# Kernel tuning notes

Hardware: AMD Instinct MI355X
Metric: run time of the kernel (lower is better)

Reference implementation:

```python
import jax, jax.numpy as jnp
import numpy as np

M_DIM = 1024
N_HEADS = 16
H_DIM = M_DIM // N_HEADS
B, S_DEC, S_ENC = 2, 2048, 2048
NEG = -1e9
LN_EPS = 1e-5


def _layernorm(x, g, b):
    mu = jnp.mean(x, axis=-1, keepdims=True)
    var = jnp.mean(jnp.square(x - mu), axis=-1, keepdims=True)
    return (x - mu) * jax.lax.rsqrt(var + LN_EPS) * g + b


def _mha(q_in, kv_in, Wq, bq, Wk, bk, Wv, bv, causal):
    # Wq/Wk/Wv: [H, m_dim, h_dim]; stacked equivalent of per-head nn.Linear
    q = jnp.einsum('bsm,hmd->bhsd', q_in, Wq) + bq[:, None, :]
    k = jnp.einsum('bsm,hmd->bhsd', kv_in, Wk) + bk[:, None, :]
    v = jnp.einsum('bsm,hmd->bhsd', kv_in, Wv) + bv[:, None, :]
    scores = jnp.einsum('bhqd,bhkd->bhqk', q, k) / jnp.sqrt(jnp.asarray(H_DIM, q.dtype))
    if causal:
        sq, sk = scores.shape[-2], scores.shape[-1]
        mask = jnp.tril(jnp.ones((sq, sk), dtype=bool))
        scores = jnp.where(mask, scores, jnp.asarray(NEG, scores.dtype))
    attn = jax.nn.softmax(scores, axis=-1)
    o = jnp.einsum('bhqk,bhkd->bhqd', attn, v)
    bsz, h, sq, d = o.shape
    # concat order: head-major along last dim, same as torch.cat over heads
    return o.transpose(0, 2, 1, 3).reshape(bsz, sq, h * d)


def setup_inputs() -> dict:
    key = jax.random.key(0)
    ks = jax.random.split(key, 32)
    s = 1.0 / np.sqrt(M_DIM)
    s2 = 1.0 / np.sqrt(2 * M_DIM)
    d = {
        'input': jax.random.normal(ks[0], (B, S_DEC, M_DIM), jnp.float32),
        'encoder_out': jax.random.normal(ks[1], (B, S_ENC, M_DIM), jnp.float32),
        # self-attention heads (stacked)
        'Wq1': jax.random.normal(ks[2], (N_HEADS, M_DIM, H_DIM), jnp.float32) * s,
        'bq1': jnp.zeros((N_HEADS, H_DIM), jnp.float32),
        'Wk1': jax.random.normal(ks[3], (N_HEADS, M_DIM, H_DIM), jnp.float32) * s,
        'bk1': jnp.zeros((N_HEADS, H_DIM), jnp.float32),
        'Wv1': jax.random.normal(ks[4], (N_HEADS, M_DIM, H_DIM), jnp.float32) * s,
        'bv1': jnp.zeros((N_HEADS, H_DIM), jnp.float32),
        'Wo1': jax.random.normal(ks[5], (M_DIM, M_DIM), jnp.float32) * s,
        'bo1': jnp.zeros((M_DIM,), jnp.float32),
        'ln1_g': jnp.ones((M_DIM,), jnp.float32),
        'ln1_b': jnp.zeros((M_DIM,), jnp.float32),
        # cross-attention heads (stacked)
        'Wq2': jax.random.normal(ks[6], (N_HEADS, M_DIM, H_DIM), jnp.float32) * s,
        'bq2': jnp.zeros((N_HEADS, H_DIM), jnp.float32),
        'Wk2': jax.random.normal(ks[7], (N_HEADS, M_DIM, H_DIM), jnp.float32) * s,
        'bk2': jnp.zeros((N_HEADS, H_DIM), jnp.float32),
        'Wv2': jax.random.normal(ks[8], (N_HEADS, M_DIM, H_DIM), jnp.float32) * s,
        'bv2': jnp.zeros((N_HEADS, H_DIM), jnp.float32),
        'Wo2': jax.random.normal(ks[9], (M_DIM, M_DIM), jnp.float32) * s,
        'bo2': jnp.zeros((M_DIM,), jnp.float32),
        'ln2_g': jnp.ones((M_DIM,), jnp.float32),
        'ln2_b': jnp.zeros((M_DIM,), jnp.float32),
        # FFN (expansion factor 2, per source)
        'W_ff1': jax.random.normal(ks[10], (M_DIM, 2 * M_DIM), jnp.float32) * s,
        'b_ff1': jnp.zeros((2 * M_DIM,), jnp.float32),
        'W_ff2': jax.random.normal(ks[11], (2 * M_DIM, M_DIM), jnp.float32) * s2,
        'b_ff2': jnp.zeros((M_DIM,), jnp.float32),
        'ln3_g': jnp.ones((M_DIM,), jnp.float32),
        'ln3_b': jnp.zeros((M_DIM,), jnp.float32),
    }
    return d


def reference(input, encoder_out,
              Wq1, bq1, Wk1, bk1, Wv1, bv1, Wo1, bo1, ln1_g, ln1_b,
              Wq2, bq2, Wk2, bk2, Wv2, bv2, Wo2, bo2, ln2_g, ln2_b,
              W_ff1, b_ff1, W_ff2, b_ff2, ln3_g, ln3_b):
    # masked self-attention (dropout = identity in eval)
    sa = _mha(input, input, Wq1, bq1, Wk1, bk1, Wv1, bv1, causal=True)
    sa = sa @ Wo1 + bo1
    out1 = _layernorm(sa + input, ln1_g, ln1_b)
    # cross-attention
    ca = _mha(out1, encoder_out, Wq2, bq2, Wk2, bk2, Wv2, bv2, causal=False)
    ca = ca @ Wo2 + bo2
    out1 = _layernorm(out1 + ca, ln2_g, ln2_b)
    # FFN
    ff = jax.nn.relu(out1 @ W_ff1 + b_ff1) @ W_ff2 + b_ff2
    out = _layernorm(ff + out1, ln3_g, ln3_b)
    return out
```

## Files before the change

### kernel.cpp

```cpp
#include <hip/hip_runtime.h>
#include <math.h>

#define B_ 2
#define S_ 2048
#define M_ 1024
#define H_ 16
#define D_ 64
#define R_ (B_*S_)

typedef __attribute__((ext_vector_type(8))) short short8v;
typedef __attribute__((ext_vector_type(4))) float float4v;

__device__ __forceinline__ float4 ld4(const float* p) {
    return *(const float4* __restrict__)p;
}

__device__ __forceinline__ ushort f2bf(float f) {
    union { float f; unsigned u; } x; x.f = f;
    unsigned u = x.u + 0x7fffu + ((x.u >> 16) & 1u);
    return (ushort)(u >> 16);
}
__device__ __forceinline__ float bf2f(ushort s) {
    union { unsigned u; float f; } x; x.u = ((unsigned)s) << 16; return x.f;
}
__device__ __forceinline__ unsigned cvtpk(float lo, float hi) {
    unsigned r;
    asm("v_cvt_pk_bf16_f32 %0, %1, %2" : "=v"(r) : "v"(lo), "v"(hi));
    return r;
}
#if __has_builtin(__builtin_amdgcn_exp2f)
__device__ __forceinline__ float fexp2(float x) { return __builtin_amdgcn_exp2f(x); }
#else
__device__ __forceinline__ float fexp2(float x) { return exp2f(x); }
#endif
#if __has_builtin(__builtin_amdgcn_rcpf)
__device__ __forceinline__ float frcp(float x) { return __builtin_amdgcn_rcpf(x); }
#else
__device__ __forceinline__ float frcp(float x) { return 1.f / x; }
#endif
__device__ __forceinline__ float4v mfma16(short8v a, short8v b, float4v c) {
    return __builtin_amdgcn_mfma_f32_16x16x32_bf16(a, b, c, 0, 0, 0);
}
__device__ __forceinline__ void glds16(const void* g, void* l) {
    __builtin_amdgcn_global_load_lds(
        (const __attribute__((address_space(1))) void*)g,
        (__attribute__((address_space(3))) void*)l, 16, 0, 0);
}

__global__ __launch_bounds__(256) void cast2_k(const float* __restrict__ a,
                                               const float* __restrict__ b,
                                               ushort* __restrict__ oa,
                                               ushort* __restrict__ ob) {
    size_t u = (size_t)blockIdx.x * 256 + threadIdx.x;
    const float* in; ushort* out;
    if (u < (1u << 20)) { in = a; out = oa; }
    else { u -= (1u << 20); in = b; out = ob; }
    float4 v = ld4(in + u * 4);
    ushort4 o = { f2bf(v.x), f2bf(v.y), f2bf(v.z), f2bf(v.w) };
    *(ushort4*)&out[u * 4] = o;
}

__global__ __launch_bounds__(256) void biasp_k(
    const float* __restrict__ q1, const float* __restrict__ k1,
    const float* __restrict__ v1, const float* __restrict__ k2,
    const float* __restrict__ v2, const float* __restrict__ q2,
    float* __restrict__ dst, float SCv) {
    const int seg = blockIdx.x >> 2;
    const int li = (blockIdx.x & 3) * 256 + threadIdx.x;
    const float* s; int off; float sc;
    switch (seg) {
        case 0: s = q1; off = 0;    sc = SCv; break;
        case 1: s = k1; off = 1024; sc = 1.f; break;
        case 2: s = v1; off = 2048; sc = 1.f; break;
        case 3: s = k2; off = 4096; sc = 1.f; break;
        case 4: s = v2; off = 5120; sc = 1.f; break;
        default: s = q2; off = 8192; sc = SCv; break;
    }
    dst[off + li] = s[li] * sc;
}

__global__ __launch_bounds__(256) void wtransH_k(
    const float* __restrict__ s0, const float* __restrict__ s1,
    const float* __restrict__ s2, const float* __restrict__ s3,
    const float* __restrict__ s4, const float* __restrict__ s5,
    ushort* __restrict__ oQKV1, ushort* __restrict__ oQ2,
    ushort* __restrict__ oKV2, float SCv) {
    __shared__ float t[32][33];
    const int z = blockIdx.z, s6 = z >> 4, h = z & 15;
    const float* srcs[6] = { s0, s1, s2, s3, s4, s5 };
    const float* ib = srcs[s6] + (size_t)h * 1024 * 64;
    ushort* ob;
    if (s6 < 3)       ob = oQKV1 + (size_t)s6 * (1024 * 1024) + (size_t)h * (64 * 1024);
    else if (s6 == 3) ob = oQ2 + (size_t)h * (64 * 1024);
    else              ob = oKV2 + (size_t)(s6 - 4) * (1024 * 1024) + (size_t)h * (64 * 1024);
    const float scale = (s6 == 0 || s6 == 3) ? SCv : 1.f;
    const int k0 = blockIdx.y * 32, n0 = blockIdx.x * 32;
    const int tx = threadIdx.x & 31, ty = threadIdx.x >> 5;
    #pragma unroll
    for (int i = 0; i < 4; ++i)
        t[ty + i * 8][tx] = ib[(size_t)(k0 + ty + i * 8) * 64 + n0 + tx];
    __syncthreads();
    #pragma unroll
    for (int i = 0; i < 4; ++i)
        ob[(size_t)(n0 + ty + i * 8) * 1024 + k0 + tx] = f2bf(t[tx][ty + i * 8] * scale);
}

__global__ __launch_bounds__(256) void wtrans_k(const float* __restrict__ inA,
                                                const float* __restrict__ inB,
                                                ushort* __restrict__ outA,
                                                ushort* __restrict__ outB,
                                                int K, int N) {
    __shared__ float t[32][33];
    const float* ib = blockIdx.z ? inB : inA;
    ushort* ob = blockIdx.z ? outB : outA;
    const int k0 = blockIdx.y * 32, n0 = blockIdx.x * 32;
    const int tx = threadIdx.x & 31, ty = threadIdx.x >> 5;
    #pragma unroll
    for (int i = 0; i < 4; ++i)
        t[ty + i * 8][tx] = ib[(size_t)(k0 + ty + i * 8) * N + n0 + tx];
    __syncthreads();
    #pragma unroll
    for (int i = 0; i < 4; ++i)
        ob[(size_t)(n0 + ty + i * 8) * K + k0 + tx] = f2bf(t[tx][ty + i * 8]);
}

template<int TM, int TN, int BK, int OUTMODE, int ACT>
__global__ __launch_bounds__(256) void gemm_bf16_k(
    const ushort* __restrict__ A, const ushort* __restrict__ Bt,
    const float* __restrict__ bias, void* __restrict__ C,
    ushort* __restrict__ Cvt, int matV, int N, int K)
{
    constexpr int NI = TM / 32;
    constexpr int NJ = TN / 32;
    constexpr int KS = BK / 32;
    constexpr int CHR = BK / 8;
    __shared__ __align__(16) ushort At[TM * BK];
    __shared__ __align__(16) ushort Bts[TN * BK];
    const int tid = threadIdx.x, lane = tid & 63, w = tid >> 6;
    const int wm = w >> 1, wn = w & 1;
    const int q = lane & 15, g = lane >> 4;
    const int m0 = blockIdx.y * TM, n0 = blockIdx.x * TN;

    float4v acc[NI][NJ];
    #pragma unroll
    for (int i = 0; i < NI; ++i)
        #pragma unroll
        for (int j = 0; j < NJ; ++j) acc[i][j] = (float4v){0.f, 0.f, 0.f, 0.f};

    for (int k0 = 0; k0 < K; k0 += BK) {
        #pragma unroll
        for (int t = 0; t < TM * CHR / 256; ++t) {
            const int cb = (w * (TM * CHR / 256) + t) * 64;
            const int c = cb + lane;
            const int row = c / CHR, kc = (c % CHR) ^ (row & (CHR - 1));
            glds16(&A[(size_t)(m0 + row) * K + k0 + kc * 8], &At[cb * 8]);
        }
        #pragma unroll
        for (int t = 0; t < TN * CHR / 256; ++t) {
            const int cb = (w * (TN * CHR / 256) + t) * 64;
            const int c = cb + lane;
            const int row = c / CHR, kc = (c % CHR) ^ (row & (CHR - 1));
            glds16(&Bt[(size_t)(n0 + row) * K + k0 + kc * 8], &Bts[cb * 8]);
        }
        __syncthreads();
        #pragma unroll
        for (int ks = 0; ks < KS; ++ks) {
            short8v af[NI], bf[NJ];
            #pragma unroll
            for (int i = 0; i < NI; ++i) {
                const int row = wm * (TM / 2) + i * 16 + q;
                af[i] = *(const short8v*)((const char*)At +
                        row * (BK * 2) + (((ks * 4 + g) ^ (q & (CHR - 1))) << 4));
            }
            #pragma unroll
            for (int j = 0; j < NJ; ++j) {
                const int row = wn * (TN / 2) + j * 16 + q;
                bf[j] = *(const short8v*)((const char*)Bts +
                        row * (BK * 2) + (((ks * 4 + g) ^ (q & (CHR - 1))) << 4));
            }
            #pragma unroll
            for (int i = 0; i < NI; ++i)
                #pragma unroll
                for (int j = 0; j < NJ; ++j)
                    acc[i][j] = mfma16(af[i], bf[j], acc[i][j]);
        }
        __syncthreads();
    }

    float bcol[NJ];
    #pragma unroll
    for (int j = 0; j < NJ; ++j) bcol[j] = bias[n0 + wn * (TN / 2) + j * 16 + q];

    #pragma unroll
    for (int i = 0; i < NI; ++i) {
        const int rowg0 = m0 + wm * (TM / 2) + i * 16 + g * 4;
        #pragma unroll
        for (int j = 0; j < NJ; ++j) {
            const int colg = n0 + wn * (TN / 2) + j * 16 + q;
            float v[4];
            #pragma unroll
            for (int r = 0; r < 4; ++r) {
                v[r] = acc[i][j][r] + bcol[j];
                if (ACT) v[r] = fmaxf(v[r], 0.f);
            }
            if (OUTMODE == 0) {
                #pragma unroll
                for (int r = 0; r < 4; ++r)
                    ((float*)C)[(size_t)(rowg0 + r) * N + colg] = v[r];
            } else if (OUTMODE == 1) {
                #pragma unroll
                for (int r = 0; r < 4; ++r)
                    ((ushort*)C)[(size_t)(rowg0 + r) * N + colg] = f2bf(v[r]);
            } else {
                const int mat = colg >> 10, h = (colg >> 6) & 15, d = colg & 63;
                const int bb = rowg0 >> 11, s0 = rowg0 & 2047;
                if (mat == matV) {
                    uint2 pv;
                    pv.x = cvtpk(v[0], v[1]);
                    pv.y = cvtpk(v[2], v[3]);
                    *(uint2*)&Cvt[((size_t)(bb * H_ + h) * D_ + d) * S_ + s0] = pv;
                } else {
                    #pragma unroll
                    for (int r = 0; r < 4; ++r)
                        ((ushort*)C)[((((size_t)(mat * B_ + bb) * H_ + h) * S_) + s0 + r) * D_ + d] = f2bf(v[r]);
                }
            }
        }
    }
}

template<int CAUSAL>
__global__ __launch_bounds__(256, 2) void fattn_k(
    const ushort* __restrict__ Qg, const ushort* __restrict__ Kg,
    const ushort* __restrict__ VTg, ushort* __restrict__ Og, int Skv)
{
    __shared__ __align__(16) ushort Kt[2][64 * 64];
    __shared__ __align__(16) ushort Vt[2][64 * 64];
    __shared__ __align__(16) ushort Pt[128 * 64];
    const int tid = threadIdx.x, lane = tid & 63, w = tid >> 6;
    const int g = lane >> 4, q = lane & 15;
    const int id = blockIdx.x;
    const int bh = id & 31;
    const int qb = CAUSAL ? (15 - (id >> 5)) : (id >> 5);
    const int q0b = qb * 128;
    const int q0w = q0b + w * 32;

    const int c0 = tid, c1 = tid + 256;
    const ushort* kS0 = Kg + ((size_t)bh * Skv + (c0 >> 3)) * 64 + (((c0 & 7) ^ ((c0 >> 3) & 7)) * 8);
    const ushort* kS1 = Kg + ((size_t)bh * Skv + (c1 >> 3)) * 64 + (((c1 & 7) ^ ((c1 >> 3) & 7)) * 8);
    const ushort* vS0 = VTg + ((size_t)bh * 64 + (c0 >> 3)) * (size_t)Skv + (((c0 & 7) ^ ((c0 >> 3) & 7)) * 8);
    const ushort* vS1 = VTg + ((size_t)bh * 64 + (c1 >> 3)) * (size_t)Skv + (((c1 & 7) ^ ((c1 >> 3) & 7)) * 8);

#define STAGE(nb) do { \
        glds16(kS0, &Kt[nb][(w * 64) * 8]); \
        glds16(kS1, &Kt[nb][(256 + w * 64) * 8]); \
        glds16(vS0, &Vt[nb][(w * 64) * 8]); \
        glds16(vS1, &Vt[nb][(256 + w * 64) * 8]); \
        kS0 += 64 * 64; kS1 += 64 * 64; vS0 += 64; vS1 += 64; } while (0)

    short8v qf[2][2];
    #pragma unroll
    for (int h2 = 0; h2 < 2; ++h2)
        #pragma unroll
        for (int kf = 0; kf < 2; ++kf)
            qf[h2][kf] = *(const short8v*)&Qg[((size_t)bh * S_ + q0w + h2 * 16 + q) * 64 + kf * 32 + g * 8];

    const int swz = (g ^ (q & 7)) << 4;
    const int ktB = q * 128 + swz;
    const int vtB = q * 128 + swz;
    const int pfB0 = (w * 32 + q) * 128 + swz;
    const int poB0 = (w * 32 + q) * 128 +
                     ((((g >> 1) ^ (q & 7)) << 4) | ((g & 1) << 3));

    float4v oacc[4][2];
    #pragma unroll
    for (int d2 = 0; d2 < 4; ++d2)
        #pragma unroll
        for (int h2 = 0; h2 < 2; ++h2) oacc[d2][h2] = (float4v){0.f, 0.f, 0.f, 0.f};
    float m_[2] = {-1e30f, -1e30f}, l_[2] = {0.f, 0.f};

    const int ktiles = CAUSAL ? (2 * qb + 2) : (Skv >> 6);
    int cur = 0;

    STAGE(0);
    __syncthreads();

    for (int kt = 0; kt < ktiles; ++kt) {
        if (kt + 1 < ktiles) STAGE(cur ^ 1);
        const char* ktp = (const char*)Kt + cur * 8192;
        const char* vtp = (const char*)Vt + cur * 8192;
        const int kv0 = kt * 64;

        float4v st[2][4];
        __builtin_amdgcn_s_setprio(1);
        #pragma unroll
        for (int kvf = 0; kvf < 4; ++kvf) {
            short8v k0 = *(const short8v*)(ktp + (ktB + kvf * 2048));
            short8v k1 = *(const short8v*)(ktp + ((ktB + kvf * 2048) ^ 64));
            #pragma unroll
            for (int h2 = 0; h2 < 2; ++h2) {
                st[h2][kvf] = mfma16(k0, qf[h2][0], (float4v){0.f, 0.f, 0.f, 0.f});
                st[h2][kvf] = mfma16(k1, qf[h2][1], st[h2][kvf]);
            }
        }
        __builtin_amdgcn_s_setprio(0);

        if (CAUSAL && kv0 + 63 > q0b) {
            #pragma unroll
            for (int h2 = 0; h2 < 2; ++h2) {
                const int qg_ = q0w + h2 * 16 + q;
                #pragma unroll
                for (int kvf = 0; kvf < 4; ++kvf)
                    #pragma unroll
                    for (int r = 0; r < 4; ++r)
                        if (kv0 + kvf * 16 + g * 4 + r > qg_) st[h2][kvf][r] = -1e9f;
            }
        }

        #pragma unroll
        for (int h2 = 0; h2 < 2; ++h2) {
            float mA[4];
            #pragma unroll
            for (int kvf = 0; kvf < 4; ++kvf)
                mA[kvf] = fmaxf(fmaxf(st[h2][kvf][0], st[h2][kvf][1]),
                                fmaxf(st[h2][kvf][2], st[h2][kvf][3]));
            float mx = fmaxf(fmaxf(mA[0], mA[1]), fmaxf(mA[2], mA[3]));
            mx = fmaxf(mx, __shfl_xor(mx, 16));
            mx = fmaxf(mx, __shfl_xor(mx, 32));

            if (!__all(mx <= m_[h2])) {
                const float nm = fmaxf(m_[h2], mx);
                const float f = fexp2(m_[h2] - nm);
                l_[h2] *= f;
                #pragma unroll
                for (int d2 = 0; d2 < 4; ++d2) oacc[d2][h2] = oacc[d2][h2] * f;
                m_[h2] = nm;
            }

            float sA[4];
            #pragma unroll
            for (int kvf = 0; kvf < 4; ++kvf) {
                #pragma unroll
                for (int r = 0; r < 4; ++r) st[h2][kvf][r] = fexp2(st[h2][kvf][r] - m_[h2]);
                sA[kvf] = (st[h2][kvf][0] + st[h2][kvf][1]) + (st[h2][kvf][2] + st[h2][kvf][3]);
            }
            l_[h2] += (sA[0] + sA[1]) + (sA[2] + sA[3]);

            #pragma unroll
            for (int kvf = 0; kvf < 4; ++kvf) {
                uint2 pv;
                pv.x = cvtpk(st[h2][kvf][0], st[h2][kvf][1]);
                pv.y = cvtpk(st[h2][kvf][2], st[h2][kvf][3]);
                *(uint2*)((char*)Pt + ((poB0 + h2 * 2048) ^ (kvf << 5))) = pv;
            }
        }

        short8v pf[2][2];
        #pragma unroll
        for (int kf = 0; kf < 2; ++kf)
            #pragma unroll
            for (int h2 = 0; h2 < 2; ++h2)
                pf[kf][h2] = *(const short8v*)((const char*)Pt + ((pfB0 + h2 * 2048) ^ (kf << 6)));
        __builtin_amdgcn_s_setprio(1);
        #pragma unroll
        for (int df = 0; df < 4; ++df) {
            #pragma unroll
            for (int kf = 0; kf < 2; ++kf) {
                short8v vfr = *(const short8v*)(vtp + ((vtB + df * 2048) ^ (kf << 6)));
                #pragma unroll
                for (int h2 = 0; h2 < 2; ++h2)
                    oacc[df][h2] = mfma16(vfr, pf[kf][h2], oacc[df][h2]);
            }
        }
        __builtin_amdgcn_s_setprio(0);

        __syncthreads();
        cur ^= 1;
    }
#undef STAGE

    #pragma unroll
    for (int h2 = 0; h2 < 2; ++h2) {
        float lr = l_[h2];
        lr += __shfl_xor(lr, 16);
        lr += __shfl_xor(lr, 32);
        const float inv = frcp(lr);
        const int qr = w * 32 + h2 * 16 + q;
        #pragma unroll
        for (int df = 0; df < 4; ++df) {
            uint2 ov;
            ov.x = cvtpk(oacc[df][h2][0] * inv, oacc[df][h2][1] * inv);
            ov.y = cvtpk(oacc[df][h2][2] * inv, oacc[df][h2][3] * inv);
            *(uint2*)((char*)Pt + qr * 128 +
                      ((((2 * df + (g >> 1)) ^ (q & 7)) << 4) | ((g & 1) << 3))) = ov;
        }
    }
    __syncthreads();
    const int b = bh >> 4, h = bh & 15;
    #pragma unroll
    for (int t = 0; t < 4; ++t) {
        const int c = t * 256 + tid;
        const int qrow = c >> 3, ch = c & 7;
        short8v v = *(const short8v*)((char*)Pt + qrow * 128 + ((ch ^ (qrow & 7)) << 4));
        *(short8v*)&Og[((size_t)(b * S_ + q0b + qrow)) * M_ + h * 64 + ch * 8] = v;
    }
}

template<int EMITB>
__global__ __launch_bounds__(256) void ln_k(
    const ushort* __restrict__ X, const float* __restrict__ Rz,
    const float* __restrict__ g, const float* __restrict__ be,
    float* __restrict__ outf, ushort* __restrict__ outb)
{
    __shared__ float red[8];
    const int row = blockIdx.x, tid = threadIdx.x;
    const int lane = tid & 63, w = tid >> 6;

    ushort4 xu = *(const ushort4*)&X[(size_t)row * M_ + tid * 4];
    float4 rr = ld4(Rz + (size_t)row * M_ + tid * 4);
    float4 x = make_float4(bf2f(xu.x) + rr.x, bf2f(xu.y) + rr.y,
                           bf2f(xu.z) + rr.z, bf2f(xu.w) + rr.w);

    float sm = x.x + x.y + x.z + x.w;
    #pragma unroll
    for (int off = 1; off < 64; off <<= 1) sm += __shfl_xor(sm, off);
    if (lane == 0) red[w] = sm;
    __syncthreads();
    const float mean = (red[0] + red[1] + red[2] + red[3]) * (1.f / M_);

    x.x -= mean; x.y -= mean; x.z -= mean; x.w -= mean;
    float vs = x.x * x.x + x.y * x.y + x.z * x.z + x.w * x.w;
    #pragma unroll
    for (int off = 1; off < 64; off <<= 1) vs += __shfl_xor(vs, off);
    if (lane == 0) red[4 + w] = vs;
    __syncthreads();
    const float var = (red[4] + red[5] + red[6] + red[7]) * (1.f / M_);
    const float rs = rsqrtf(var + 1e-5f);

    float4 gg = ld4(g + tid * 4), bb = ld4(be + tid * 4);
    float4 y = make_float4(x.x * rs * gg.x + bb.x, x.y * rs * gg.y + bb.y,
                           x.z * rs * gg.z + bb.z, x.w * rs * gg.w + bb.w);
    *(float4*)(outf + (size_t)row * M_ + tid * 4) = y;
    if (EMITB) {
        ushort4 ob = { f2bf(y.x), f2bf(y.y), f2bf(y.z), f2bf(y.w) };
        *(ushort4*)&outb[(size_t)row * M_ + tid * 4] = ob;
    }
}

extern "C" void kernel_launch(void* const* d_in, const int* in_sizes, int n_in,
                              void* d_out, int out_size, void* d_ws, size_t ws_size,
                              hipStream_t stream)
{
    const float* input = (const float*)d_in[0];
    const float* enc   = (const float*)d_in[1];
    const float* Wq1 = (const float*)d_in[2];  const float* bq1 = (const float*)d_in[3];
    const float* Wk1 = (const float*)d_in[4];  const float* bk1 = (const float*)d_in[5];
    const float* Wv1 = (const float*)d_in[6];  const float* bv1 = (const float*)d_in[7];
    const float* Wo1 = (const float*)d_in[8];  const float* bo1 = (const float*)d_in[9];
    const float* ln1g = (const float*)d_in[10]; const float* ln1b = (const float*)d_in[11];
    const float* Wq2 = (const float*)d_in[12]; const float* bq2 = (const float*)d_in[13];
    const float* Wk2 = (const float*)d_in[14]; const float* bk2 = (const float*)d_in[15];
    const float* Wv2 = (const float*)d_in[16]; const float* bv2 = (const float*)d_in[17];
    const float* Wo2 = (const float*)d_in[18]; const float* bo2 = (const float*)d_in[19];
    const float* ln2g = (const float*)d_in[20]; const float* ln2b = (const float*)d_in[21];
    const float* Wf1 = (const float*)d_in[22]; const float* bf1 = (const float*)d_in[23];
    const float* Wf2 = (const float*)d_in[24]; const float* bf2 = (const float*)d_in[25];
    const float* ln3g = (const float*)d_in[26]; const float* ln3b = (const float*)d_in[27];

    const float SC = 0.18033688011112042f;

    char* W = (char*)d_ws;
    #define OFS(mb) ((void*)(W + (size_t)(mb) * 1024 * 1024))
    ushort* x0b    = (ushort*)OFS(0);
    ushort* encb   = (ushort*)OFS(8);
    ushort* WqkvT1 = (ushort*)OFS(16);
    ushort* Wo1T   = (ushort*)OFS(22);
    ushort* Wq2T   = (ushort*)OFS(24);
    ushort* WkvT2  = (ushort*)OFS(26);
    ushort* Wo2T   = (ushort*)OFS(30);
    ushort* Wf1T   = (ushort*)OFS(32);
    ushort* Wf2T   = (ushort*)OFS(36);
    float*  biasQKV1 = (float*)OFS(40);
    float*  biasKV2  = (float*)((char*)OFS(40) + 16384);
    float*  biasQ2   = (float*)((char*)OFS(40) + 32768);
    ushort* QKV1   = (ushort*)OFS(41);
    ushort* VT1    = (ushort*)OFS(65);
    ushort* att1b  = (ushort*)OFS(73);
    ushort* o1b    = (ushort*)OFS(81);
    float*  out1f  = (float*)OFS(41);
    ushort* out1b  = (ushort*)OFS(57);
    ushort* Q2     = (ushort*)OFS(65);
    ushort* KV2    = (ushort*)OFS(73);
    ushort* VT2    = (ushort*)OFS(0);
    ushort* att2b  = (ushort*)OFS(8);
    ushort* o2b    = (ushort*)OFS(65);
    float*  out2f  = (float*)OFS(73);
    ushort* out2b  = (ushort*)OFS(0);
    ushort* ff1b   = (ushort*)OFS(41);
    ushort* ff2b   = (ushort*)OFS(57);
    float*  out    = (float*)d_out;
    const size_t MAT = (size_t)B_ * H_ * S_ * D_;

    dim3 blk(256);

    cast2_k<<<8192, blk, 0, stream>>>(input, enc, x0b, encb);
    biasp_k<<<24, blk, 0, stream>>>(bq1, bk1, bv1, bk2, bv2, bq2, biasQKV1, SC);
    wtransH_k<<<dim3(2, 32, 96), blk, 0, stream>>>(Wq1, Wk1, Wv1, Wq2, Wk2, Wv2,
                                                   WqkvT1, Wq2T, WkvT2, SC);
    wtrans_k<<<dim3(32, 32, 2), blk, 0, stream>>>(Wo1, Wo2, Wo1T, Wo2T, 1024, 1024);
    wtrans_k<<<dim3(64, 32, 1), blk, 0, stream>>>(Wf1, Wf1, Wf1T, Wf1T, 1024, 2048);
    wtrans_k<<<dim3(32, 64, 1), blk, 0, stream>>>(Wf2, Wf2, Wf2T, Wf2T, 2048, 1024);

    gemm_bf16_k<128, 128, 64, 2, 0><<<dim3(24, 32), blk, 0, stream>>>(
        x0b, WqkvT1, biasQKV1, QKV1, VT1, 2, 3072, 1024);
    fattn_k<1><<<dim3(512), blk, 0, stream>>>(QKV1, QKV1 + MAT, VT1, att1b, S_);
    gemm_bf16_k<64, 64, 64, 1, 0><<<dim3(16, 64), blk, 0, stream>>>(
        att1b, Wo1T, bo1, o1b, nullptr, 9, 1024, 1024);
    ln_k<1><<<dim3(R_), blk, 0, stream>>>(o1b, input, ln1g, ln1b, out1f, out1b);

    gemm_bf16_k<64, 64, 64, 2, 0><<<dim3(16, 64), blk, 0, stream>>>(
        out1b, Wq2T, biasQ2, Q2, nullptr, 9, 1024, 1024);
    gemm_bf16_k<128, 128, 64, 2, 0><<<dim3(16, 32), blk, 0, stream>>>(
        encb, WkvT2, biasKV2, KV2, VT2, 1, 2048, 1024);
    fattn_k<0><<<dim3(512), blk, 0, stream>>>(Q2, KV2, VT2, att2b, S_);
    gemm_bf16_k<64, 64, 64, 1, 0><<<dim3(16, 64), blk, 0, stream>>>(
        att2b, Wo2T, bo2, o2b, nullptr, 9, 1024, 1024);
    ln_k<1><<<dim3(R_), blk, 0, stream>>>(o2b, out1f, ln2g, ln2b, out2f, out2b);

    gemm_bf16_k<128, 64, 64, 1, 1><<<dim3(32, 32), blk, 0, stream>>>(
        out2b, Wf1T, bf1, ff1b, nullptr, 9, 2048, 1024);
    gemm_bf16_k<64, 64, 64, 1, 0><<<dim3(16, 64), blk, 0, stream>>>(
        ff1b, Wf2T, bf2, ff2b, nullptr, 9, 1024, 2048);
    ln_k<0><<<dim3(R_), blk, 0, stream>>>(ff2b, out2f, ln3g, ln3b, out, nullptr);
    #undef OFS
}
```

Measured before the change: 315.7 us.

## Split attention KV range across two blocks and merge partials in combine kernel

Each attention query tile is now processed by two blocks covering disjoint halves of the key range (balanced causal split), writing unnormalized bf16 partial outputs plus row max/sum, and a new combine kernel merges them with softmax rescaling. This doubles the grid to 1024 blocks to fill the GPU better, and occupancy is raised to 3 waves per SIMD. The cross-attention KV projection GEMM is moved earlier, and workspace buffers are reshuffled. It adds extra memory traffic and a launch for the combine step, and storing the unnormalized partials in bf16 may cost some precision.

```diff
diff --git a/kernel.cpp b/kernel.cpp
--- a/kernel.cpp
+++ b/kernel.cpp
@@ -230,9 +230,10 @@
 }
 
 template<int CAUSAL>
-__global__ __launch_bounds__(256, 2) void fattn_k(
+__global__ __launch_bounds__(256, 3) void fattn_k(
     const ushort* __restrict__ Qg, const ushort* __restrict__ Kg,
-    const ushort* __restrict__ VTg, ushort* __restrict__ Og, int Skv)
+    const ushort* __restrict__ VTg, ushort* __restrict__ Opart,
+    float2* __restrict__ mlOut, int Skv)
 {
     __shared__ __align__(16) ushort Kt[2][64 * 64];
     __shared__ __align__(16) ushort Vt[2][64 * 64];
@@ -241,15 +242,19 @@
     const int g = lane >> 4, q = lane & 15;
     const int id = blockIdx.x;
     const int bh = id & 31;
-    const int qb = CAUSAL ? (15 - (id >> 5)) : (id >> 5);
+    const int t_ = (id >> 5) & 15;
+    const int half = id >> 9;
+    const int qb = CAUSAL ? ((t_ < 8) ? (15 - t_) : (t_ - 8)) : t_;
     const int q0b = qb * 128;
     const int q0w = q0b + w * 32;
+    const int t0k = CAUSAL ? (half ? (qb + 1) : 0) : (half * 16);
+    const int t1k = CAUSAL ? (half ? (2 * qb + 2) : (qb + 1)) : (half * 16 + 16);
 
     const int c0 = tid, c1 = tid + 256;
-    const ushort* kS0 = Kg + ((size_t)bh * Skv + (c0 >> 3)) * 64 + (((c0 & 7) ^ ((c0 >> 3) & 7)) * 8);
-    const ushort* kS1 = Kg + ((size_t)bh * Skv + (c1 >> 3)) * 64 + (((c1 & 7) ^ ((c1 >> 3) & 7)) * 8);
-    const ushort* vS0 = VTg + ((size_t)bh * 64 + (c0 >> 3)) * (size_t)Skv + (((c0 & 7) ^ ((c0 >> 3) & 7)) * 8);
-    const ushort* vS1 = VTg + ((size_t)bh * 64 + (c1 >> 3)) * (size_t)Skv + (((c1 & 7) ^ ((c1 >> 3) & 7)) * 8);
+    const ushort* kS0 = Kg + ((size_t)bh * Skv + t0k * 64 + (c0 >> 3)) * 64 + (((c0 & 7) ^ ((c0 >> 3) & 7)) * 8);
+    const ushort* kS1 = Kg + ((size_t)bh * Skv + t0k * 64 + (c1 >> 3)) * 64 + (((c1 & 7) ^ ((c1 >> 3) & 7)) * 8);
+    const ushort* vS0 = VTg + ((size_t)bh * 64 + (c0 >> 3)) * (size_t)Skv + t0k * 64 + (((c0 & 7) ^ ((c0 >> 3) & 7)) * 8);
+    const ushort* vS1 = VTg + ((size_t)bh * 64 + (c1 >> 3)) * (size_t)Skv + t0k * 64 + (((c1 & 7) ^ ((c1 >> 3) & 7)) * 8);
 
 #define STAGE(nb) do { \
         glds16(kS0, &Kt[nb][(w * 64) * 8]); \
@@ -279,14 +284,12 @@
         for (int h2 = 0; h2 < 2; ++h2) oacc[d2][h2] = (float4v){0.f, 0.f, 0.f, 0.f};
     float m_[2] = {-1e30f, -1e30f}, l_[2] = {0.f, 0.f};
 
-    const int ktiles = CAUSAL ? (2 * qb + 2) : (Skv >> 6);
     int cur = 0;
-
     STAGE(0);
     __syncthreads();
 
-    for (int kt = 0; kt < ktiles; ++kt) {
-        if (kt + 1 < ktiles) STAGE(cur ^ 1);
+    for (int kt = t0k; kt < t1k; ++kt) {
+        if (kt + 1 < t1k) STAGE(cur ^ 1);
         const char* ktp = (const char*)Kt + cur * 8192;
         const char* vtp = (const char*)Vt + cur * 8192;
         const int kv0 = kt * 64;
@@ -384,26 +387,55 @@
         float lr = l_[h2];
         lr += __shfl_xor(lr, 16);
         lr += __shfl_xor(lr, 32);
-        const float inv = frcp(lr);
         const int qr = w * 32 + h2 * 16 + q;
+        if (g == 0) mlOut[(size_t)id * 128 + qr] = make_float2(m_[h2], lr);
         #pragma unroll
         for (int df = 0; df < 4; ++df) {
             uint2 ov;
-            ov.x = cvtpk(oacc[df][h2][0] * inv, oacc[df][h2][1] * inv);
-            ov.y = cvtpk(oacc[df][h2][2] * inv, oacc[df][h2][3] * inv);
+            ov.x = cvtpk(oacc[df][h2][0], oacc[df][h2][1]);
+            ov.y = cvtpk(oacc[df][h2][2], oacc[df][h2][3]);
             *(uint2*)((char*)Pt + qr * 128 +
                       ((((2 * df + (g >> 1)) ^ (q & 7)) << 4) | ((g & 1) << 3))) = ov;
         }
     }
     __syncthreads();
-    const int b = bh >> 4, h = bh & 15;
     #pragma unroll
     for (int t = 0; t < 4; ++t) {
         const int c = t * 256 + tid;
         const int qrow = c >> 3, ch = c & 7;
         short8v v = *(const short8v*)((char*)Pt + qrow * 128 + ((ch ^ (qrow & 7)) << 4));
-        *(short8v*)&Og[((size_t)(b * S_ + q0b + qrow)) * M_ + h * 64 + ch * 8] = v;
-    }
+        *(short8v*)&Opart[(size_t)id * 8192 + qrow * 64 + ch * 8] = v;
+    }
+}
+
+template<int CAUSAL>
+__global__ __launch_bounds__(256) void fcomb_k(
+    const ushort* __restrict__ Opart, const float2* __restrict__ ml,
+    ushort* __restrict__ att)
+{
+    const int it = blockIdx.x * 256 + threadIdx.x;
+    const int seg = it & 7;
+    const int qrow = (it >> 3) & 127;
+    const int qb = (it >> 10) & 15;
+    const int bh = it >> 14;
+    const int t0 = CAUSAL ? ((qb >= 8) ? (15 - qb) : (qb + 8)) : qb;
+    const int id0 = bh + 32 * t0;
+    const int id1 = id0 + 512;
+    const float2 ml0 = ml[id0 * 128 + qrow];
+    const float2 ml1 = ml[id1 * 128 + qrow];
+    const float m = fmaxf(ml0.x, ml1.x);
+    const float e0 = fexp2(ml0.x - m), e1 = fexp2(ml1.x - m);
+    const float inv = frcp(e0 * ml0.y + e1 * ml1.y);
+    const float s0 = e0 * inv, s1 = e1 * inv;
+    short8v o0 = *(const short8v*)&Opart[(size_t)id0 * 8192 + qrow * 64 + seg * 8];
+    short8v o1 = *(const short8v*)&Opart[(size_t)id1 * 8192 + qrow * 64 + seg * 8];
+    union { ushort u[8]; short8v v; } r;
+    #pragma unroll
+    for (int i = 0; i < 8; ++i)
+        r.u[i] = f2bf(bf2f((ushort)o0[i]) * s0 + bf2f((ushort)o1[i]) * s1);
+    const int b = bh >> 4, h = bh & 15;
+    const int qg = qb * 128 + qrow;
+    *(short8v*)&att[((size_t)(b * S_ + qg)) * M_ + h * 64 + seg * 8] = r.v;
 }
 
 template<int EMITB>
@@ -483,21 +515,25 @@
     float*  biasQKV1 = (float*)OFS(40);
     float*  biasKV2  = (float*)((char*)OFS(40) + 16384);
     float*  biasQ2   = (float*)((char*)OFS(40) + 32768);
-    ushort* QKV1   = (ushort*)OFS(41);
-    ushort* VT1    = (ushort*)OFS(65);
-    ushort* att1b  = (ushort*)OFS(73);
-    ushort* o1b    = (ushort*)OFS(81);
+    ushort* Q1     = (ushort*)OFS(41);
+    ushort* VT1    = (ushort*)OFS(57);
+    ushort* K2     = (ushort*)OFS(65);
+    ushort* VT2    = (ushort*)OFS(73);
+    ushort* Opart1 = (ushort*)OFS(0);
+    float2* ml1    = (float2*)OFS(81);
+    ushort* att1b  = (ushort*)OFS(82);
+    ushort* o1b    = (ushort*)OFS(90);
     float*  out1f  = (float*)OFS(41);
     ushort* out1b  = (ushort*)OFS(57);
-    ushort* Q2     = (ushort*)OFS(65);
-    ushort* KV2    = (ushort*)OFS(73);
-    ushort* VT2    = (ushort*)OFS(0);
-    ushort* att2b  = (ushort*)OFS(8);
+    ushort* Q2     = (ushort*)OFS(0);
+    ushort* Opart2 = (ushort*)OFS(82);
+    float2* ml2    = (float2*)OFS(8);
+    ushort* att2b  = (ushort*)OFS(0);
     ushort* o2b    = (ushort*)OFS(65);
-    float*  out2f  = (float*)OFS(73);
-    ushort* out2b  = (ushort*)OFS(0);
+    float*  out2f  = (float*)OFS(82);
+    ushort* out2b  = (ushort*)OFS(73);
     ushort* ff1b   = (ushort*)OFS(41);
-    ushort* ff2b   = (ushort*)OFS(57);
+    ushort* ff2b   = (ushort*)OFS(0);
     float*  out    = (float*)d_out;
     const size_t MAT = (size_t)B_ * H_ * S_ * D_;
 
@@ -512,17 +548,20 @@
     wtrans_k<<<dim3(32, 64, 1), blk, 0, stream>>>(Wf2, Wf2, Wf2T, Wf2T, 2048, 1024);
 
     gemm_bf16_k<128, 128, 64, 2, 0><<<dim3(24, 32), blk, 0, stream>>>(
-        x0b, WqkvT1, biasQKV1, QKV1, VT1, 2, 3072, 1024);
-    fattn_k<1><<<dim3(512), blk, 0, stream>>>(QKV1, QKV1 + MAT, VT1, att1b, S_);
+        x0b, WqkvT1, biasQKV1, Q1, VT1, 2, 3072, 1024);
+    gemm_bf16_k<128, 128, 64, 2, 0><<<dim3(16, 32), blk, 0, stream>>>(
+        encb, WkvT2, biasKV2, K2, VT2, 1, 2048, 1024);
+
+    fattn_k<1><<<dim3(1024), blk, 0, stream>>>(Q1, Q1 + MAT, VT1, Opart1, ml1, S_);
+    fcomb_k<1><<<dim3(2048), blk, 0, stream>>>(Opart1, ml1, att1b);
     gemm_bf16_k<64, 64, 64, 1, 0><<<dim3(16, 64), blk, 0, stream>>>(
         att1b, Wo1T, bo1, o1b, nullptr, 9, 1024, 1024);
     ln_k<1><<<dim3(R_), blk, 0, stream>>>(o1b, input, ln1g, ln1b, out1f, out1b);
 
     gemm_bf16_k<64, 64, 64, 2, 0><<<dim3(16, 64), blk, 0, stream>>>(
         out1b, Wq2T, biasQ2, Q2, nullptr, 9, 1024, 1024);
-    gemm_bf16_k<128, 128, 64, 2, 0><<<dim3(16, 32), blk, 0, stream>>>(
-        encb, WkvT2, biasKV2, KV2, VT2, 1, 2048, 1024);
-    fattn_k<0><<<dim3(512), blk, 0, stream>>>(Q2, KV2, VT2, att2b, S_);
+    fattn_k<0><<<dim3(1024), blk, 0, stream>>>(Q2, K2, VT2, Opart2, ml2, S_);
+    fcomb_k<0><<<dim3(2048), blk, 0, stream>>>(Opart2, ml2, att2b);
     gemm_bf16_k<64, 64, 64, 1, 0><<<dim3(16, 64), blk, 0, stream>>>(
         att2b, Wo2T, bo2, o2b, nullptr, 9, 1024, 1024);
     ln_k<1><<<dim3(R_), blk, 0, stream>>>(o2b, out1f, ln2g, ln2b, out2f, out2b);
```

New measurement: 317.1 us. Within noise of the previous version (+0.4%).

## Switch flash attention to 32x32 MFMA with register-shuffled P, drop LDS P buffer

Applied to the files above, without the earlier changes.

Rewrites the attention inner loop to use 32x32x16 bf16 MFMAs, so each wave holds one 32-row query tile as a single accumulator. The P matrix is rearranged into B-operand layout with cross-half lane shuffles instead of a round trip through shared memory, which removes the P LDS buffer. The smaller LDS footprint allows three blocks per CU, and causal block ordering is changed to interleave long and short query tiles for load balance. The risks are higher register pressure from the 16-wide accumulators under the tighter launch bound, and the extra shuffle instructions.

```diff
diff --git a/kernel.cpp b/kernel.cpp
--- a/kernel.cpp
+++ b/kernel.cpp
@@ -10,6 +10,7 @@
 
 typedef __attribute__((ext_vector_type(8))) short short8v;
 typedef __attribute__((ext_vector_type(4))) float float4v;
+typedef __attribute__((ext_vector_type(16))) float float16v;
 
 __device__ __forceinline__ float4 ld4(const float* p) {
     return *(const float4* __restrict__)p;
@@ -40,6 +41,9 @@
 #endif
 __device__ __forceinline__ float4v mfma16(short8v a, short8v b, float4v c) {
     return __builtin_amdgcn_mfma_f32_16x16x32_bf16(a, b, c, 0, 0, 0);
+}
+__device__ __forceinline__ float16v mfma32(short8v a, short8v b, float16v c) {
+    return __builtin_amdgcn_mfma_f32_32x32x16_bf16(a, b, c, 0, 0, 0);
 }
 __device__ __forceinline__ void glds16(const void* g, void* l) {
     __builtin_amdgcn_global_load_lds(
@@ -230,18 +234,18 @@
 }
 
 template<int CAUSAL>
-__global__ __launch_bounds__(256, 2) void fattn_k(
+__global__ __launch_bounds__(256, 3) void fattn_k(
     const ushort* __restrict__ Qg, const ushort* __restrict__ Kg,
     const ushort* __restrict__ VTg, ushort* __restrict__ Og, int Skv)
 {
     __shared__ __align__(16) ushort Kt[2][64 * 64];
     __shared__ __align__(16) ushort Vt[2][64 * 64];
-    __shared__ __align__(16) ushort Pt[128 * 64];
     const int tid = threadIdx.x, lane = tid & 63, w = tid >> 6;
-    const int g = lane >> 4, q = lane & 15;
+    const int q = lane & 31, hi = lane >> 5;
     const int id = blockIdx.x;
     const int bh = id & 31;
-    const int qb = CAUSAL ? (15 - (id >> 5)) : (id >> 5);
+    const int t_ = id >> 5;
+    const int qb = CAUSAL ? ((t_ < 8) ? (15 - t_) : (t_ - 8)) : t_;
     const int q0b = qb * 128;
     const int q0w = q0b + w * 32;
 
@@ -258,26 +262,17 @@
         glds16(vS1, &Vt[nb][(256 + w * 64) * 8]); \
         kS0 += 64 * 64; kS1 += 64 * 64; vS0 += 64; vS1 += 64; } while (0)
 
-    short8v qf[2][2];
-    #pragma unroll
-    for (int h2 = 0; h2 < 2; ++h2)
-        #pragma unroll
-        for (int kf = 0; kf < 2; ++kf)
-            qf[h2][kf] = *(const short8v*)&Qg[((size_t)bh * S_ + q0w + h2 * 16 + q) * 64 + kf * 32 + g * 8];
-
-    const int swz = (g ^ (q & 7)) << 4;
-    const int ktB = q * 128 + swz;
-    const int vtB = q * 128 + swz;
-    const int pfB0 = (w * 32 + q) * 128 + swz;
-    const int poB0 = (w * 32 + q) * 128 +
-                     ((((g >> 1) ^ (q & 7)) << 4) | ((g & 1) << 3));
-
-    float4v oacc[4][2];
-    #pragma unroll
-    for (int d2 = 0; d2 < 4; ++d2)
-        #pragma unroll
-        for (int h2 = 0; h2 < 2; ++h2) oacc[d2][h2] = (float4v){0.f, 0.f, 0.f, 0.f};
-    float m_[2] = {-1e30f, -1e30f}, l_[2] = {0.f, 0.f};
+    short8v qf[4];
+    #pragma unroll
+    for (int ki = 0; ki < 4; ++ki)
+        qf[ki] = *(const short8v*)&Qg[((size_t)bh * S_ + q0w + q) * 64 + ki * 16 + hi * 8];
+
+    const int ktB = q * 128 + ((hi ^ (q & 7)) << 4);
+
+    float16v oacc0, oacc1;
+    #pragma unroll
+    for (int r = 0; r < 16; ++r) { oacc0[r] = 0.f; oacc1[r] = 0.f; }
+    float m_ = -1e30f, l_ = 0.f;
 
     const int ktiles = CAUSAL ? (2 * qb + 2) : (Skv >> 6);
     int cur = 0;
@@ -291,86 +286,92 @@
         const char* vtp = (const char*)Vt + cur * 8192;
         const int kv0 = kt * 64;
 
-        float4v st[2][4];
+        float16v st0, st1;
+        #pragma unroll
+        for (int r = 0; r < 16; ++r) { st0[r] = 0.f; st1[r] = 0.f; }
         __builtin_amdgcn_s_setprio(1);
         #pragma unroll
-        for (int kvf = 0; kvf < 4; ++kvf) {
-            short8v k0 = *(const short8v*)(ktp + (ktB + kvf * 2048));
-            short8v k1 = *(const short8v*)(ktp + ((ktB + kvf * 2048) ^ 64));
-            #pragma unroll
-            for (int h2 = 0; h2 < 2; ++h2) {
-                st[h2][kvf] = mfma16(k0, qf[h2][0], (float4v){0.f, 0.f, 0.f, 0.f});
-                st[h2][kvf] = mfma16(k1, qf[h2][1], st[h2][kvf]);
+        for (int ki = 0; ki < 4; ++ki) {
+            short8v kf0 = *(const short8v*)(ktp + (ktB ^ (ki << 5)));
+            short8v kf1 = *(const short8v*)(ktp + (ktB ^ (ki << 5)) + 4096);
+            st0 = mfma32(kf0, qf[ki], st0);
+            st1 = mfma32(kf1, qf[ki], st1);
+        }
+        __builtin_amdgcn_s_setprio(0);
+
+        if (CAUSAL && kv0 + 63 > q0b) {
+            const int qg_ = q0w + q;
+            #pragma unroll
+            for (int r = 0; r < 16; ++r) {
+                const int row = (r & 3) + 8 * (r >> 2) + 4 * hi;
+                if (kv0 + row > qg_)      st0[r] = -1e9f;
+                if (kv0 + 32 + row > qg_) st1[r] = -1e9f;
             }
         }
-        __builtin_amdgcn_s_setprio(0);
-
-        if (CAUSAL && kv0 + 63 > q0b) {
-            #pragma unroll
-            for (int h2 = 0; h2 < 2; ++h2) {
-                const int qg_ = q0w + h2 * 16 + q;
-                #pragma unroll
-                for (int kvf = 0; kvf < 4; ++kvf)
-                    #pragma unroll
-                    for (int r = 0; r < 4; ++r)
-                        if (kv0 + kvf * 16 + g * 4 + r > qg_) st[h2][kvf][r] = -1e9f;
+
+        float tm[16];
+        #pragma unroll
+        for (int r = 0; r < 16; ++r) tm[r] = fmaxf(st0[r], st1[r]);
+        #pragma unroll
+        for (int off = 8; off >= 1; off >>= 1)
+            #pragma unroll
+            for (int i = 0; i < 8; ++i)
+                if (i < off) tm[i] = fmaxf(tm[i], tm[i + off]);
+        float mx = fmaxf(tm[0], __shfl_xor(tm[0], 32));
+
+        if (!__all(mx <= m_)) {
+            const float nm = fmaxf(m_, mx);
+            const float f = fexp2(m_ - nm);
+            l_ *= f;
+            oacc0 = oacc0 * f;
+            oacc1 = oacc1 * f;
+            m_ = nm;
+        }
+
+        float ts[16];
+        #pragma unroll
+        for (int r = 0; r < 16; ++r) {
+            st0[r] = fexp2(st0[r] - m_);
+            st1[r] = fexp2(st1[r] - m_);
+            ts[r] = st0[r] + st1[r];
+        }
+        #pragma unroll
+        for (int off = 8; off >= 1; off >>= 1)
+            #pragma unroll
+            for (int i = 0; i < 8; ++i)
+                if (i < off) ts[i] += ts[i + off];
+        l_ += ts[0] + __shfl_xor(ts[0], 32);
+
+        unsigned W0[8], W1[8];
+        #pragma unroll
+        for (int s = 0; s < 8; ++s) {
+            W0[s] = cvtpk(st0[2 * s], st0[2 * s + 1]);
+            W1[s] = cvtpk(st1[2 * s], st1[2 * s + 1]);
+        }
+
+        short8v bq[4];
+        #pragma unroll
+        for (int kb = 0; kb < 4; ++kb) {
+            union { unsigned u[4]; short8v v; } bb;
+            #pragma unroll
+            for (int j = 0; j < 4; ++j) {
+                const unsigned* Wb = (kb >> 1) ? W1 : W0;
+                const int s0 = (j & 1) + 4 * (kb & 1);
+                const unsigned own  = hi ? Wb[s0 + 2] : Wb[s0];
+                const unsigned send = hi ? Wb[s0]     : Wb[s0 + 2];
+                const unsigned rec  = (unsigned)__shfl_xor((int)send, 32);
+                bb.u[j] = (j >> 1) ? (hi ? own : rec) : (hi ? rec : own);
             }
-        }
-
-        #pragma unroll
-        for (int h2 = 0; h2 < 2; ++h2) {
-            float mA[4];
-            #pragma unroll
-            for (int kvf = 0; kvf < 4; ++kvf)
-                mA[kvf] = fmaxf(fmaxf(st[h2][kvf][0], st[h2][kvf][1]),
-                                fmaxf(st[h2][kvf][2], st[h2][kvf][3]));
-            float mx = fmaxf(fmaxf(mA[0], mA[1]), fmaxf(mA[2], mA[3]));
-            mx = fmaxf(mx, __shfl_xor(mx, 16));
-            mx = fmaxf(mx, __shfl_xor(mx, 32));
-
-            if (!__all(mx <= m_[h2])) {
-                const float nm = fmaxf(m_[h2], mx);
-                const float f = fexp2(m_[h2] - nm);
-                l_[h2] *= f;
-                #pragma unroll
-                for (int d2 = 0; d2 < 4; ++d2) oacc[d2][h2] = oacc[d2][h2] * f;
-                m_[h2] = nm;
-            }
-
-            float sA[4];
-            #pragma unroll
-            for (int kvf = 0; kvf < 4; ++kvf) {
-                #pragma unroll
-                for (int r = 0; r < 4; ++r) st[h2][kvf][r] = fexp2(st[h2][kvf][r] - m_[h2]);
-                sA[kvf] = (st[h2][kvf][0] + st[h2][kvf][1]) + (st[h2][kvf][2] + st[h2][kvf][3]);
-            }
-            l_[h2] += (sA[0] + sA[1]) + (sA[2] + sA[3]);
-
-            #pragma unroll
-            for (int kvf = 0; kvf < 4; ++kvf) {
-                uint2 pv;
-                pv.x = cvtpk(st[h2][kvf][0], st[h2][kvf][1]);
-                pv.y = cvtpk(st[h2][kvf][2], st[h2][kvf][3]);
-                *(uint2*)((char*)Pt + ((poB0 + h2 * 2048) ^ (kvf << 5))) = pv;
-            }
-        }
-
-        short8v pf[2][2];
-        #pragma unroll
-        for (int kf = 0; kf < 2; ++kf)
-            #pragma unroll
-            for (int h2 = 0; h2 < 2; ++h2)
-                pf[kf][h2] = *(const short8v*)((const char*)Pt + ((pfB0 + h2 * 2048) ^ (kf << 6)));
+            bq[kb] = bb.v;
+        }
+
         __builtin_amdgcn_s_setprio(1);
         #pragma unroll
-        for (int df = 0; df < 4; ++df) {
-            #pragma unroll
-            for (int kf = 0; kf < 2; ++kf) {
-                short8v vfr = *(const short8v*)(vtp + ((vtB + df * 2048) ^ (kf << 6)));
-                #pragma unroll
-                for (int h2 = 0; h2 < 2; ++h2)
-                    oacc[df][h2] = mfma16(vfr, pf[kf][h2], oacc[df][h2]);
-            }
+        for (int kb = 0; kb < 4; ++kb) {
+            short8v vf0 = *(const short8v*)(vtp + (ktB ^ (kb << 5)));
+            short8v vf1 = *(const short8v*)(vtp + (ktB ^ (kb << 5)) + 4096);
+            oacc0 = mfma32(vf0, bq[kb], oacc0);
+            oacc1 = mfma32(vf1, bq[kb], oacc1);
         }
         __builtin_amdgcn_s_setprio(0);
 
@@ -379,21 +380,17 @@
     }
 #undef STAGE
 
-    #pragma unroll
-    for (int h2 = 0; h2 < 2; ++h2) {
-        float lr = l_[h2];
-        lr += __shfl_xor(lr, 16);
-        lr += __shfl_xor(lr, 32);
-        const float inv = frcp(lr);
-        const int qr = w * 32 + h2 * 16 + q;
-        #pragma unroll
-        for (int df = 0; df < 4; ++df) {
-            uint2 ov;
-            ov.x = cvtpk(oacc[df][h2][0] * inv, oacc[df][h2][1] * inv);
-            ov.y = cvtpk(oacc[df][h2][2] * inv, oacc[df][h2][3] * inv);
-            *(uint2*)((char*)Pt + qr * 128 +
-                      ((((2 * df + (g >> 1)) ^ (q & 7)) << 4) | ((g & 1) << 3))) = ov;
-        }
+    const float inv = frcp(l_);
+    char* Ob = (char*)Kt;
+    const int qr = w * 32 + q;
+    #pragma unroll
+    for (int s = 0; s < 8; ++s) {
+        const int d0a = 2 * (s & 1) + 8 * (s >> 1) + 4 * hi;
+        unsigned wa = cvtpk(oacc0[2 * s] * inv, oacc0[2 * s + 1] * inv);
+        *(unsigned*)(Ob + qr * 128 + ((((d0a >> 3) ^ (qr & 7)) << 4) | ((2 * d0a) & 15))) = wa;
+        const int d0b = d0a + 32;
+        unsigned wb = cvtpk(oacc1[2 * s] * inv, oacc1[2 * s + 1] * inv);
+        *(unsigned*)(Ob + qr * 128 + ((((d0b >> 3) ^ (qr & 7)) << 4) | ((2 * d0b) & 15))) = wb;
     }
     __syncthreads();
     const int b = bh >> 4, h = bh & 15;
@@ -401,7 +398,7 @@
     for (int t = 0; t < 4; ++t) {
         const int c = t * 256 + tid;
         const int qrow = c >> 3, ch = c & 7;
-        short8v v = *(const short8v*)((char*)Pt + qrow * 128 + ((ch ^ (qrow & 7)) << 4));
+        short8v v = *(const short8v*)(Ob + qrow * 128 + ((ch ^ (qrow & 7)) << 4));
         *(short8v*)&Og[((size_t)(b * S_ + q0b + qrow)) * M_ + h * 64 + ch * 8] = v;
     }
 }
```

Measured after the change: 315.7 us. Within noise of the previous version (-0.0%).
